# Kernel optimization log

Hardware: AMD Instinct MI355X
Metric: run time of the kernel (lower is better)

The kernel has to match this reference:

```python
import jax, jax.numpy as jnp
import numpy as np


def _ln(x, w, b):
    m = x.mean(-1, keepdims=True)
    v = ((x - m) ** 2).mean(-1, keepdims=True)
    return (x - m) * jax.lax.rsqrt(v + 1e-5) * w + b


def _l2n(x):
    return x / jnp.clip(jnp.linalg.norm(x, axis=-1, keepdims=True), 1e-12, None)


def _forward(tokens, emb, ln1_w, ln1_b, wq, wkv, wo, wo_b, knn_scale,
             ln2_w, ln2_b, ff_w1, ff_b1, ff_w2, ff_b2, lnf_w, lnf_b,
             w_logits, b_logits, xl_mems, db_kv, knn_layer, topk):
    B, N = tokens.shape
    depth = wq.shape[0]
    H = knn_scale.shape[0]
    Dh = wkv.shape[-1] // 2
    XL = xl_mems.shape[2]
    NEG = jnp.finfo(emb.dtype).max
    x = emb[tokens]  # [B,N,dim]
    # causal mask with XL-cache offset: triu(j - i + 1)
    causal = jnp.triu(jnp.ones((N, N + XL), bool), XL + 1)
    for l in range(depth):
        h = _ln(x, ln1_w[l], ln1_b[l])
        q = (h @ wq[l]).reshape(B, N, H, Dh).transpose(0, 2, 1, 3)  # [B,H,N,Dh]
        kv = h @ wkv[l]
        k, v = kv[..., :Dh], kv[..., Dh:]  # single shared kv head [B,N,Dh]
        is_knn = (l == knn_layer)
        if is_knn:
            q, k = _l2n(q), _l2n(k)
            scale = jnp.exp(knn_scale)[None, :, None, None]
        else:
            q = q * (Dh ** -0.5)
            scale = 1.0
        k = jnp.concatenate((xl_mems[l, :, :, 0], k), axis=1)  # [B,N+XL,Dh]
        v = jnp.concatenate((xl_mems[l, :, :, 1], v), axis=1)
        sim = jnp.einsum('bhid,bjd->bhij', q, k) * scale
        sim = jnp.where(causal, -NEG, sim)
        if is_knn:
            dbk = _l2n(db_kv[..., 0, :])  # [B,M,Dh] stored keys are l2-normalized
            dbv = db_kv[..., 1, :]
            simdb = jnp.einsum('bhid,bmd->bhim', q, dbk)
            _, idx = jax.lax.top_k(simdb, topk)  # [B,H,N,topk] inner-product KNN
            mem_k = jax.vmap(lambda t, i: t[i])(dbk, idx)  # [B,H,N,topk,Dh]
            mem_v = jax.vmap(lambda t, i: t[i])(dbv, idx)
            sim_mem = jnp.einsum('bhid,bhijd->bhij', q, mem_k) * scale
            attn = jax.nn.softmax(jnp.concatenate((sim_mem, sim), axis=-1), axis=-1)
            mem_attn, loc_attn = attn[..., :topk], attn[..., topk:]
            out = (jnp.einsum('bhij,bjd->bhid', loc_attn, v)
                   + jnp.einsum('bhij,bhijd->bhid', mem_attn, mem_v))
        else:
            attn = jax.nn.softmax(sim, axis=-1)
            out = jnp.einsum('bhij,bjd->bhid', attn, v)
        out = out.transpose(0, 2, 1, 3).reshape(B, N, H * Dh)
        x = out @ wo[l] + wo_b[l] + x
        h = _ln(x, ln2_w[l], ln2_b[l])
        x = jax.nn.gelu(h @ ff_w1[l] + ff_b1[l], approximate=False) @ ff_w2[l] + ff_b2[l] + x
    return _ln(x, lnf_w, lnf_b) @ w_logits + b_logits


def setup_inputs() -> dict:
    B, N, DIM, H, DH, DEPTH, V, XL, M = 2, 1024, 1024, 16, 64, 4, 32000, 256, 4096
    key = jax.random.key(0)
    ks = jax.random.split(key, 12)
    s = 0.02
    rn = lambda k, sh: (jax.random.normal(k, sh) * s).astype(jnp.float32)
    return dict(
        tokens=jax.random.randint(ks[0], (B, N), 0, V, dtype=jnp.int32),
        emb=rn(ks[1], (V, DIM)),
        ln1_w=jnp.ones((DEPTH, DIM), jnp.float32), ln1_b=jnp.zeros((DEPTH, DIM), jnp.float32),
        wq=rn(ks[2], (DEPTH, DIM, H * DH)),
        wkv=rn(ks[3], (DEPTH, DIM, 2 * DH)),
        wo=rn(ks[4], (DEPTH, H * DH, DIM)), wo_b=jnp.zeros((DEPTH, DIM), jnp.float32),
        knn_scale=jnp.full((H,), float(np.log(20.0)), jnp.float32),
        ln2_w=jnp.ones((DEPTH, DIM), jnp.float32), ln2_b=jnp.zeros((DEPTH, DIM), jnp.float32),
        ff_w1=rn(ks[5], (DEPTH, DIM, 4 * DIM)), ff_b1=jnp.zeros((DEPTH, 4 * DIM), jnp.float32),
        ff_w2=rn(ks[6], (DEPTH, 4 * DIM, DIM)), ff_b2=jnp.zeros((DEPTH, DIM), jnp.float32),
        lnf_w=jnp.ones((DIM,), jnp.float32), lnf_b=jnp.zeros((DIM,), jnp.float32),
        w_logits=rn(ks[7], (DIM, V)), b_logits=jnp.zeros((V,), jnp.float32),
        xl_mems=jax.random.normal(ks[8], (DEPTH, B, XL, 2, DH), jnp.float32),
        db_kv=jax.random.normal(ks[9], (B, M, 2, DH), jnp.float32),
        knn_layer=2, topk=32,
    )


def reference(tokens, emb, ln1_w, ln1_b, wq, wkv, wo, wo_b, knn_scale,
              ln2_w, ln2_b, ff_w1, ff_b1, ff_w2, ff_b2, lnf_w, lnf_b,
              w_logits, b_logits, xl_mems, db_kv, knn_layer, topk):
    return _forward(tokens, emb, ln1_w, ln1_b, wq, wkv, wo, wo_b, knn_scale,
                    ln2_w, ln2_b, ff_w1, ff_b1, ff_w2, ff_b2, lnf_w, lnf_b,
                    w_logits, b_logits, xl_mems, db_kv, knn_layer, topk)
```

## Files before the change

### kernel.cpp

```cpp
#include <hip/hip_runtime.h>
#include <hip/hip_bf16.h>
#include <math.h>

#define BB 2
#define NSEQ 1024
#define DIM 1024
#define NH 16
#define DH 64
#define DEPTH 4
#define VOCAB 32000
#define XLM 256
#define MDB 4096
#define TOPK 32
#define KNN_LAYER 2
#define BNROWS (BB * NSEQ)
#define LOGITS_CHUNK 6400
#define NKEYS 1280
#define KSP_PS ((size_t)BB * NKEYS * DH)

typedef __bf16 bf16x8v __attribute__((ext_vector_type(8)));
typedef float f32x4v __attribute__((ext_vector_type(4)));
typedef unsigned short u16x8v __attribute__((ext_vector_type(8)));

__device__ __forceinline__ float bfbits2f(unsigned short u) {
    union { float f; unsigned int i; } v; v.i = ((unsigned int)u) << 16; return v.f;
}
__device__ __forceinline__ unsigned short f2bfbits(float f) {
    union { __hip_bfloat16 b; unsigned short u; } v;
    v.b = __float2bfloat16(f);
    return v.u;
}
__device__ __forceinline__ float bf2f(__hip_bfloat16 h) { return __bfloat162float(h); }
__device__ __forceinline__ __hip_bfloat16 f2bf(float f) { return __float2bfloat16(f); }

__device__ __forceinline__ void gload16(const void* gp, void* lp) {
    __builtin_amdgcn_global_load_lds(
        (const __attribute__((address_space(1))) unsigned int*)gp,
        (__attribute__((address_space(3))) unsigned int*)lp, 16, 0, 0);
}

__global__ __launch_bounds__(256) void embed_kernel(const int* __restrict__ tok,
                                                    const float* __restrict__ emb,
                                                    float* __restrict__ x) {
    int r = blockIdx.x, t = threadIdx.x;
    int id = tok[r];
    const float* er = emb + (size_t)id * DIM;
    float* xr = x + (size_t)r * DIM;
#pragma unroll
    for (int i = 0; i < 4; i++) xr[t + 256 * i] = er[t + 256 * i];
}

__global__ __launch_bounds__(256) void ln_kernel(const float* __restrict__ x,
                                                 const float* __restrict__ w,
                                                 const float* __restrict__ b,
                                                 __hip_bfloat16* __restrict__ y,
                                                 size_t ypS) {
    __shared__ float red[256];
    int r = blockIdx.x, t = threadIdx.x;
    const float* xr = x + (size_t)r * DIM;
    float v[4];
#pragma unroll
    for (int i = 0; i < 4; i++) v[i] = xr[t + 256 * i];
    float s = v[0] + v[1] + v[2] + v[3];
    red[t] = s; __syncthreads();
    for (int st = 128; st; st >>= 1) { if (t < st) red[t] += red[t + st]; __syncthreads(); }
    float mean = red[0] * (1.0f / DIM);
    __syncthreads();
    float s2 = 0.f;
#pragma unroll
    for (int i = 0; i < 4; i++) { float d = v[i] - mean; s2 += d * d; }
    red[t] = s2; __syncthreads();
    for (int st = 128; st; st >>= 1) { if (t < st) red[t] += red[t + st]; __syncthreads(); }
    float rs = rsqrtf(red[0] * (1.0f / DIM) + 1e-5f);
    __hip_bfloat16* yr = y + (size_t)r * DIM;
#pragma unroll
    for (int i = 0; i < 4; i++) {
        int c = t + 256 * i;
        float val = (v[i] - mean) * rs * w[c] + b[c];
        __hip_bfloat16 hv = f2bf(val);
        yr[c] = hv;
        yr[c + ypS] = f2bf(val - bf2f(hv));
    }
}

__global__ void l2norm_kernel(float* __restrict__ p, int stride) {
    int r = blockIdx.x, t = threadIdx.x;
    float* pr = p + (size_t)r * stride;
    float v = pr[t];
    float s = v * v;
#pragma unroll
    for (int off = 32; off; off >>= 1) s += __shfl_xor(s, off, 64);
    float n = fmaxf(sqrtf(s), 1e-12f);
    pr[t] = v / n;
}

__global__ void dbnorm_kernel(const float* __restrict__ db, float* __restrict__ dbkn) {
    int r = blockIdx.x, t = threadIdx.x;
    float v = db[((size_t)r * 2 + 0) * DH + t];
    float s = v * v;
#pragma unroll
    for (int off = 32; off; off >>= 1) s += __shfl_xor(s, off, 64);
    float n = fmaxf(sqrtf(s), 1e-12f);
    dbkn[(size_t)r * DH + t] = v / n;
}

__global__ __launch_bounds__(256) void split_conv(const float* __restrict__ x,
                                                  unsigned short* __restrict__ y,
                                                  size_t pS, size_t n4) {
    size_t idx = (size_t)blockIdx.x * 256 + threadIdx.x;
    if (idx >= n4) return;
    float4 v = *(const float4*)&x[idx * 4];
    float vv[4] = {v.x, v.y, v.z, v.w};
    ushort4 h4, l4;
    unsigned short* hp = (unsigned short*)&h4;
    unsigned short* lp = (unsigned short*)&l4;
#pragma unroll
    for (int j = 0; j < 4; j++) {
        hp[j] = f2bfbits(vv[j]);
        lp[j] = f2bfbits(vv[j] - bfbits2f(hp[j]));
    }
    *(ushort4*)&y[idx * 4] = h4;
    *(ushort4*)&y[idx * 4 + pS] = l4;
}

template <int NP>
__global__ __launch_bounds__(256) void combine_k(const float* __restrict__ pbuf, size_t pS,
                                                 float* __restrict__ out,
                                                 const float* __restrict__ bias,
                                                 const float* __restrict__ res,
                                                 int N, size_t n4) {
    size_t idx = (size_t)blockIdx.x * 256 + threadIdx.x;
    if (idx >= n4) return;
    f32x4v s = *(const f32x4v*)&pbuf[idx * 4];
#pragma unroll
    for (int z = 1; z < NP; z++) {
        f32x4v v = *(const f32x4v*)&pbuf[(size_t)z * pS + idx * 4];
        s += v;
    }
    if (bias) {
        int col = (int)((idx * 4) % (size_t)N);
        const f32x4v bv = *(const f32x4v*)&bias[col];
        s += bv;
    }
    if (res) {
        f32x4v r = *(const f32x4v*)&res[idx * 4];
        s += r;
    }
    *(f32x4v*)&out[idx * 4] = s;
}

__global__ void kv_prep(const float* __restrict__ kvf, const float* __restrict__ xlm,
                        unsigned short* __restrict__ ksp, unsigned short* __restrict__ vtp) {
    int key = blockIdx.x, b = blockIdx.y, d = threadIdx.x;
    float kvv, vvv;
    if (key < XLM) {
        kvv = xlm[(((size_t)b * XLM + key) * 2 + 0) * DH + d];
        vvv = xlm[(((size_t)b * XLM + key) * 2 + 1) * DH + d];
    } else {
        const float* r = &kvf[(size_t)(b * NSEQ + key - XLM) * 128];
        kvv = r[d]; vvv = r[64 + d];
    }
    unsigned short kh = f2bfbits(kvv), kl = f2bfbits(kvv - bfbits2f(kh));
    unsigned short vh = f2bfbits(vvv), vl = f2bfbits(vvv - bfbits2f(vh));
    size_t ko = (size_t)b * NKEYS * DH + (size_t)key * DH + d;
    ksp[ko] = kh; ksp[ko + KSP_PS] = kl;
    size_t vo = (size_t)b * DH * NKEYS + (size_t)d * NKEYS + key;
    vtp[vo] = vh; vtp[vo + KSP_PS] = vl;
}

__global__ __launch_bounds__(256) void wconv(const float* __restrict__ W,
                                             __hip_bfloat16* __restrict__ WT,
                                             size_t wpS, int K, int N, int ldw,
                                             int wlo) {
    __shared__ float tile[64][65];
    int k0 = blockIdx.x * 64, n0 = blockIdx.y * 64;
    int t = threadIdx.x;
    int r = t >> 4, c4 = (t & 15) * 4;
#pragma unroll
    for (int rr = 0; rr < 4; rr++) {
        int row = rr * 16 + r;
        float4 v = *(const float4*)&W[(size_t)(k0 + row) * ldw + n0 + c4];
        tile[row][c4] = v.x; tile[row][c4 + 1] = v.y; tile[row][c4 + 2] = v.z; tile[row][c4 + 3] = v.w;
    }
    __syncthreads();
#pragma unroll
    for (int rr = 0; rr < 4; rr++) {
        int nrow = rr * 16 + r;
        size_t base = (size_t)(n0 + nrow) * K + k0 + c4;
#pragma unroll
        for (int j = 0; j < 4; j++) {
            float val = tile[c4 + j][nrow];
            __hip_bfloat16 hv = f2bf(val);
            WT[base + j] = hv;
            if (wlo) WT[base + j + wpS] = f2bf(val - bf2f(hv));
        }
    }
}

template <typename OT, int ACT, int TERMS, int MODE>
__global__ __launch_bounds__(256) void gemm_split(const __hip_bfloat16* __restrict__ A, int lda, size_t apS,
                                                  const __hip_bfloat16* __restrict__ BT, int ldb, size_t bpS,
                                                  OT* __restrict__ C, int ldc, size_t cpS, int K,
                                                  const float* __restrict__ bias,
                                                  const float* __restrict__ res,
                                                  int bh0) {
    __shared__ __align__(16) __hip_bfloat16 sAh[128 * 32];
    __shared__ __align__(16) __hip_bfloat16 sBh[128 * 32];
    __shared__ __align__(16) __hip_bfloat16 sAl[TERMS >= 2 ? 128 * 32 : 1];
    __shared__ __align__(16) __hip_bfloat16 sBl[TERMS >= 3 ? 128 * 32 : 1];
    if constexpr (MODE == 1) {
        int bh = bh0 + blockIdx.z;
        A += ((size_t)(bh >> 4) * NSEQ) * lda + (bh & 15) * DH;
        BT += (size_t)(bh >> 4) * MDB * ldb;
        C += (size_t)blockIdx.z * NSEQ * ldc;
    }
    if constexpr (MODE == 2) {
        A += (size_t)blockIdx.z * K;
        BT += (size_t)blockIdx.z * K;
        C += (size_t)blockIdx.z * cpS;
    }
    int bn = blockIdx.x * 128;
    int bm = blockIdx.y * 128;
    int t = threadIdx.x;
    int lane = t & 63, wid = t >> 6;
    int wr = wid >> 1, wc = wid & 1;
    int lr = lane & 15, kc = lane >> 4;

    f32x4v acc[4][4];
#pragma unroll
    for (int m = 0; m < 4; m++)
#pragma unroll
        for (int n = 0; n < 4; n++) acc[m][n] = (f32x4v){0.f, 0.f, 0.f, 0.f};

    for (int k0 = 0; k0 < K; k0 += 32) {
        __syncthreads();
#pragma unroll
        for (int it = 0; it < 2; it++) {
            int e = wid * 128 + it * 64 + lane;
            int r = e >> 2;
            int cl = (e & 3) ^ ((r >> 1) & 3);
            size_t aoff = (size_t)(bm + r) * lda + k0 + cl * 8;
            size_t boff = (size_t)(bn + r) * ldb + k0 + cl * 8;
            int dst = (wid * 128 + it * 64) * 8;
            gload16(&A[aoff], &sAh[dst]);
            gload16(&BT[boff], &sBh[dst]);
            if constexpr (TERMS >= 2) gload16(&A[aoff + apS], &sAl[dst]);
            if constexpr (TERMS >= 3) gload16(&BT[boff + bpS], &sBl[dst]);
        }
        __syncthreads();

        bf16x8v ah[4], al[4], bh[4], bl[4];
#pragma unroll
        for (int m = 0; m < 4; m++) {
            int row = wr * 64 + m * 16 + lr;
            int off = row * 32 + ((kc ^ ((row >> 1) & 3)) << 3);
            ah[m] = *(const bf16x8v*)&sAh[off];
            if constexpr (TERMS >= 2) al[m] = *(const bf16x8v*)&sAl[off];
        }
#pragma unroll
        for (int n = 0; n < 4; n++) {
            int row = wc * 64 + n * 16 + lr;
            int off = row * 32 + ((kc ^ ((row >> 1) & 3)) << 3);
            bh[n] = *(const bf16x8v*)&sBh[off];
            if constexpr (TERMS >= 3) bl[n] = *(const bf16x8v*)&sBl[off];
        }
#pragma unroll
        for (int m = 0; m < 4; m++)
#pragma unroll
            for (int n = 0; n < 4; n++) {
                acc[m][n] = __builtin_amdgcn_mfma_f32_16x16x32_bf16(ah[m], bh[n], acc[m][n], 0, 0, 0);
                if constexpr (TERMS >= 2)
                    acc[m][n] = __builtin_amdgcn_mfma_f32_16x16x32_bf16(al[m], bh[n], acc[m][n], 0, 0, 0);
                if constexpr (TERMS >= 3)
                    acc[m][n] = __builtin_amdgcn_mfma_f32_16x16x32_bf16(ah[m], bl[n], acc[m][n], 0, 0, 0);
            }
    }

#pragma unroll
    for (int m = 0; m < 4; m++) {
#pragma unroll
        for (int n = 0; n < 4; n++) {
            int gcol = bn + wc * 64 + n * 16 + lr;
            float bv = bias ? bias[gcol] : 0.f;
#pragma unroll
            for (int j = 0; j < 4; j++) {
                int grow = bm + wr * 64 + m * 16 + kc * 4 + j;
                float v = acc[m][n][j] + bv;
                if (ACT == 1) v = 0.5f * v * (1.0f + erff(v * 0.70710678118654752f));
                if (res) v += res[(size_t)grow * ldc + gcol];
                size_t idx = (size_t)grow * ldc + gcol;
                if constexpr (__is_same(OT, float)) {
                    C[idx] = v;
                } else if constexpr (__is_same(OT, unsigned short)) {
                    C[idx] = f2bfbits(v);
                } else {
                    __hip_bfloat16 hv = f2bf(v);
                    C[idx] = hv;
                    C[idx + cpS] = f2bf(v - bf2f(hv));
                }
            }
        }
    }
}

template <int KNNL>
__global__ __launch_bounds__(256) void flash_kernel(const float* __restrict__ q,
                                                    const unsigned short* __restrict__ ksp,
                                                    const unsigned short* __restrict__ vtp,
                                                    const float* __restrict__ knn_scale,
                                                    __hip_bfloat16* __restrict__ out,
                                                    size_t opS,
                                                    float* __restrict__ stats) {
    __shared__ __align__(16) unsigned short sKh[64 * 64];
    __shared__ __align__(16) unsigned short sKl[64 * 64];
    __shared__ __align__(16) unsigned short sVh[64 * 64];
    __shared__ __align__(16) unsigned short sVl[64 * 64];
    __shared__ __align__(16) float sPf[4 * 16 * 64];

    int qt = blockIdx.x, h = blockIdx.y, b = blockIdx.z;
    int q0 = qt * 64;
    int t = threadIdx.x;
    int w = t >> 6;
    int lane = t & 63;
    int lr = lane & 15, kc = lane >> 4;
    int wbase = w * 1024;

    float scale = KNNL ? __expf(knn_scale[h]) : 0.125f;

    bf16x8v qh[2], ql[2];
    {
        const float* qbase = q + (size_t)(b * NSEQ + q0 + w * 16 + lr) * DIM + h * DH;
#pragma unroll
        for (int ks = 0; ks < 2; ks++) {
            const float* s = qbase + ks * 32 + kc * 8;
            float4 a = *(const float4*)s;
            float4 c2 = *(const float4*)(s + 4);
            float vv[8] = {a.x, a.y, a.z, a.w, c2.x, c2.y, c2.z, c2.w};
            u16x8v hi, lo;
#pragma unroll
            for (int j = 0; j < 8; j++) {
                hi[j] = f2bfbits(vv[j]);
                lo[j] = f2bfbits(vv[j] - bfbits2f(hi[j]));
            }
            qh[ks] = *(bf16x8v*)&hi;
            ql[ks] = *(bf16x8v*)&lo;
        }
    }

    float m[4], l[4];
    f32x4v o[4];
#pragma unroll
    for (int j = 0; j < 4; j++) { m[j] = -1e30f; l[j] = 0.f; }
#pragma unroll
    for (int f = 0; f < 4; f++) o[f] = (f32x4v){0.f, 0.f, 0.f, 0.f};

    int ntiles = 5 + qt;
    size_t kbase = (size_t)b * NKEYS * DH;
    size_t vbase = (size_t)b * DH * NKEYS;

    for (int T = 0; T < ntiles; T++) {
        __syncthreads();
#pragma unroll
        for (int i2 = 0; i2 < 2; i2++) {
            int cbase = i2 * 256 + w * 64;
            int c = cbase + lane;
            int key = c >> 3, ch = (c & 7) ^ (key & 7);
            size_t ko = kbase + (size_t)(T * 64 + key) * DH + ch * 8;
            gload16(&ksp[ko], &sKh[cbase * 8]);
            gload16(&ksp[ko + KSP_PS], &sKl[cbase * 8]);
            int dim = c >> 3, k8 = (c & 7) ^ (dim & 7);
            size_t vo = vbase + (size_t)dim * NKEYS + T * 64 + k8 * 8;
            gload16(&vtp[vo], &sVh[cbase * 8]);
            gload16(&vtp[vo + KSP_PS], &sVl[cbase * 8]);
        }
        __syncthreads();

        f32x4v s4[4];
#pragma unroll
        for (int n = 0; n < 4; n++) s4[n] = (f32x4v){0.f, 0.f, 0.f, 0.f};
#pragma unroll
        for (int ks = 0; ks < 2; ks++) {
            bf16x8v qh_ = qh[ks], ql_ = ql[ks];
#pragma unroll
            for (int n = 0; n < 4; n++) {
                int row = n * 16 + lr;
                int off = row * 64 + (((ks * 4 + kc) ^ (lr & 7)) << 3);
                bf16x8v kh = *(const bf16x8v*)&sKh[off];
                bf16x8v kl = *(const bf16x8v*)&sKl[off];
                s4[n] = __builtin_amdgcn_mfma_f32_16x16x32_bf16(qh_, kh, s4[n], 0, 0, 0);
                s4[n] = __builtin_amdgcn_mfma_f32_16x16x32_bf16(ql_, kh, s4[n], 0, 0, 0);
                s4[n] = __builtin_amdgcn_mfma_f32_16x16x32_bf16(qh_, kl, s4[n], 0, 0, 0);
            }
        }

#pragma unroll
        for (int n = 0; n < 4; n++) {
            int key = T * 64 + n * 16 + lr;
#pragma unroll
            for (int j = 0; j < 4; j++) {
                int gq = q0 + w * 16 + kc * 4 + j;
                float sv = s4[n][j] * scale;
                s4[n][j] = (key <= XLM + gq) ? sv : -1e30f;
            }
        }

        float tm[4];
#pragma unroll
        for (int j = 0; j < 4; j++) {
            float v = fmaxf(fmaxf(s4[0][j], s4[1][j]), fmaxf(s4[2][j], s4[3][j]));
            v = fmaxf(v, __shfl_xor(v, 1, 64));
            v = fmaxf(v, __shfl_xor(v, 2, 64));
            v = fmaxf(v, __shfl_xor(v, 4, 64));
            v = fmaxf(v, __shfl_xor(v, 8, 64));
            tm[j] = v;
        }
        float alpha[4];
#pragma unroll
        for (int j = 0; j < 4; j++) {
            float mnew = fmaxf(m[j], tm[j]);
            alpha[j] = __expf(m[j] - mnew);
            m[j] = mnew;
        }
        float psum[4] = {0.f, 0.f, 0.f, 0.f};
#pragma unroll
        for (int n = 0; n < 4; n++)
#pragma unroll
            for (int j = 0; j < 4; j++) {
                float p = __expf(s4[n][j] - m[j]);
                s4[n][j] = p;
                psum[j] += p;
            }
#pragma unroll
        for (int j = 0; j < 4; j++) {
            float v = psum[j];
            v += __shfl_xor(v, 1, 64);
            v += __shfl_xor(v, 2, 64);
            v += __shfl_xor(v, 4, 64);
            v += __shfl_xor(v, 8, 64);
            l[j] = l[j] * alpha[j] + v;
        }
#pragma unroll
        for (int f = 0; f < 4; f++)
#pragma unroll
            for (int j = 0; j < 4; j++) o[f][j] *= alpha[j];

#pragma unroll
        for (int n = 0; n < 4; n++) {
            int chunkcol = 2 * n + (lr >> 3);
#pragma unroll
            for (int j = 0; j < 4; j++) {
                int row = kc * 4 + j;
                int off = wbase + row * 64 + (((chunkcol ^ (row & 7)) << 3) + (lr & 7));
                sPf[off] = s4[n][j];
            }
        }

#pragma unroll
        for (int ks = 0; ks < 2; ks++) {
            int poff = wbase + lr * 64 + (((ks * 4 + kc) ^ (lr & 7)) << 3);
            float4 a = *(const float4*)&sPf[poff];
            float4 c2 = *(const float4*)&sPf[poff + 4];
            float vv[8] = {a.x, a.y, a.z, a.w, c2.x, c2.y, c2.z, c2.w};
            u16x8v hib, lob;
#pragma unroll
            for (int j = 0; j < 8; j++) {
                hib[j] = f2bfbits(vv[j]);
                lob[j] = f2bfbits(vv[j] - bfbits2f(hib[j]));
            }
            bf16x8v ph = *(bf16x8v*)&hib;
            bf16x8v pl = *(bf16x8v*)&lob;
#pragma unroll
            for (int f = 0; f < 4; f++) {
                int row = f * 16 + lr;
                int off = row * 64 + (((ks * 4 + kc) ^ (lr & 7)) << 3);
                bf16x8v vh = *(const bf16x8v*)&sVh[off];
                bf16x8v vl = *(const bf16x8v*)&sVl[off];
                o[f] = __builtin_amdgcn_mfma_f32_16x16x32_bf16(ph, vh, o[f], 0, 0, 0);
                o[f] = __builtin_amdgcn_mfma_f32_16x16x32_bf16(pl, vh, o[f], 0, 0, 0);
                o[f] = __builtin_amdgcn_mfma_f32_16x16x32_bf16(ph, vl, o[f], 0, 0, 0);
            }
        }
    }

    float inv[4];
#pragma unroll
    for (int j = 0; j < 4; j++) inv[j] = 1.0f / l[j];
    unsigned short* outu = (unsigned short*)out;
#pragma unroll
    for (int f = 0; f < 4; f++)
#pragma unroll
        for (int j = 0; j < 4; j++) {
            int gq = q0 + w * 16 + kc * 4 + j;
            size_t oidx = (size_t)(b * NSEQ + gq) * DIM + h * DH + f * 16 + lr;
            float v = o[f][j] * inv[j];
            unsigned short hv = f2bfbits(v);
            outu[oidx] = hv;
            outu[oidx + opS] = f2bfbits(v - bfbits2f(hv));
        }
    if (KNNL && lr == 0) {
#pragma unroll
        for (int j = 0; j < 4; j++) {
            int gq = q0 + w * 16 + kc * 4 + j;
            size_t srow = (((size_t)b * NH + h) * NSEQ + gq) * 2;
            stats[srow] = m[j];
            stats[srow + 1] = l[j];
        }
    }
}

__global__ __launch_bounds__(256) void knn_select(const unsigned short* __restrict__ simdb,
                                                  const float* __restrict__ db,
                                                  const float* __restrict__ qf,
                                                  const float* __restrict__ dbkn,
                                                  const float* __restrict__ knn_scale,
                                                  const float* __restrict__ stats,
                                                  __hip_bfloat16* __restrict__ out,
                                                  size_t opS,
                                                  int bh0) {
    __shared__ unsigned short sv[4 * 4096];

    int bh = bh0 + blockIdx.y;
    int b = bh >> 4, h = bh & 15;
    int t = threadIdx.x;
    int w = t >> 6, lane = t & 63;
    int i = blockIdx.x * 4 + w;
    unsigned short* svw = &sv[w * 4096];

    const unsigned short* srow = &simdb[((size_t)blockIdx.y * NSEQ + i) * MDB];
#pragma unroll
    for (int it = 0; it < 8; it++) {
        int g = it * 64 + lane;
        int c = g >> 3, sub = g & 7;
        u16x8v d = *(const u16x8v*)&srow[(size_t)g * 8];
        *(u16x8v*)&svw[c * 64 + ((sub ^ (c & 7)) << 3)] = d;
    }

    float lmax = -1e30f; int lidx = 0;
#pragma unroll
    for (int c = 0; c < 64; c++) {
        float v = bfbits2f(svw[c * 64 + (lane ^ ((c & 7) << 3))]);
        if (v > lmax) { lmax = v; lidx = c * 64 + lane; }
    }

    int tidx = 0;
    for (int it = 0; it < TOPK; it++) {
        float v = lmax; int idx = lidx;
#pragma unroll
        for (int off = 32; off; off >>= 1) {
            float v2 = __shfl_xor(v, off, 64);
            int i2 = __shfl_xor(idx, off, 64);
            if (v2 > v || (v2 == v && i2 < idx)) { v = v2; idx = i2; }
        }
        if (lane == it) tidx = idx;
        int col = idx & 63, cc = idx >> 6;
        if (lane == 0) svw[cc * 64 + (col ^ ((cc & 7) << 3))] = 0xFF80;
        float rv = bfbits2f(svw[lane * 64 + (col ^ ((lane & 7) << 3))]);
        int ridx = lane * 64 + col;
#pragma unroll
        for (int off = 32; off; off >>= 1) {
            float v2 = __shfl_xor(rv, off, 64);
            int i2 = __shfl_xor(ridx, off, 64);
            if (v2 > rv || (v2 == rv && i2 < ridx)) { rv = v2; ridx = i2; }
        }
        if (lane == col) { lmax = rv; lidx = ridx; }
    }

    float srec = -1e30f;
    if (lane < TOPK) {
        const float* qrow = &qf[(size_t)(b * NSEQ + i) * DIM + h * DH];
        const float* krow = &dbkn[((size_t)b * MDB + tidx) * DH];
        float s = 0.f;
#pragma unroll
        for (int d4 = 0; d4 < 16; d4++) {
            float4 a = *(const float4*)&qrow[d4 * 4];
            float4 k2 = *(const float4*)&krow[d4 * 4];
            s += a.x * k2.x + a.y * k2.y + a.z * k2.z + a.w * k2.w;
        }
        srec = s;
    }

    float scl = __expf(knn_scale[h]);
    size_t srow_idx = (((size_t)b * NH + h) * NSEQ + i) * 2;
    float m_loc = stats[srow_idx], l_loc = stats[srow_idx + 1];
    float mm = srec;
#pragma unroll
    for (int off = 32; off; off >>= 1) mm = fmaxf(mm, __shfl_xor(mm, off, 64));
    float M = fmaxf(m_loc, mm * scl);
    float co = __expf(m_loc - M);
    float e = (lane < TOPK) ? __expf(srec * scl - M) : 0.f;
    float esum = e;
#pragma unroll
    for (int off = 32; off; off >>= 1) esum += __shfl_xor(esum, off, 64);
    float denom = l_loc * co + esum;

    float acc = 0.f;
#pragma unroll
    for (int j = 0; j < TOPK; j++) {
        int idxj = __shfl(tidx, j, 64);
        float ej = __shfl(e, j, 64);
        acc += ej * db[(((size_t)b * MDB + idxj) * 2 + 1) * DH + lane];
    }

    size_t op = (size_t)(b * NSEQ + i) * DIM + h * DH + lane;
    float o_loc = bf2f(out[op]) + bf2f(out[op + opS]);
    float nv = (o_loc * l_loc * co + acc) / denom;
    __hip_bfloat16 hv = f2bf(nv);
    out[op] = hv;
    out[op + opS] = f2bf(nv - bf2f(hv));
}

extern "C" void kernel_launch(void* const* d_in, const int* in_sizes, int n_in,
                              void* d_out, int out_size, void* d_ws, size_t ws_size,
                              hipStream_t stream) {
    const int* tokens = (const int*)d_in[0];
    const float* emb = (const float*)d_in[1];
    const float* ln1_w = (const float*)d_in[2];
    const float* ln1_b = (const float*)d_in[3];
    const float* wq = (const float*)d_in[4];
    const float* wkv = (const float*)d_in[5];
    const float* wo = (const float*)d_in[6];
    const float* wo_b = (const float*)d_in[7];
    const float* knn_scale = (const float*)d_in[8];
    const float* ln2_w = (const float*)d_in[9];
    const float* ln2_b = (const float*)d_in[10];
    const float* ff_w1 = (const float*)d_in[11];
    const float* ff_b1 = (const float*)d_in[12];
    const float* ff_w2 = (const float*)d_in[13];
    const float* ff_b2 = (const float*)d_in[14];
    const float* lnf_w = (const float*)d_in[15];
    const float* lnf_b = (const float*)d_in[16];
    const float* w_logits = (const float*)d_in[17];
    const float* b_logits = (const float*)d_in[18];
    const float* xl_mems = (const float*)d_in[19];
    const float* db_kv = (const float*)d_in[20];

    const size_t PS_H = (size_t)BNROWS * DIM;
    char* p = (char*)d_ws;
    float* x = (float*)p;                p += PS_H * 4;
    __hip_bfloat16* hb = (__hip_bfloat16*)p;  p += PS_H * 2 * 2;
    float* qf = (float*)p;               p += PS_H * 4;
    float* kvf = (float*)p;              p += (size_t)BNROWS * 128 * 4;
    float* dbkn = (float*)p;             p += (size_t)BB * MDB * DH * 4;
    float* stats = (float*)p;            p += (size_t)BB * NH * NSEQ * 2 * 4;
    unsigned short* ksp = (unsigned short*)p; p += KSP_PS * 2 * 2;
    unsigned short* vtp = (unsigned short*)p; p += KSP_PS * 2 * 2;
    __hip_bfloat16* wT = (__hip_bfloat16*)p; p += (size_t)4096 * DIM * 2 * 2;

    unsigned short* qsplit = (unsigned short*)wT;
    unsigned short* dbks = (unsigned short*)wT + 2 * PS_H;
    const size_t PS_DB = (size_t)BB * MDB * DH;

    const size_t PS_MID = (size_t)BNROWS * 4 * DIM;
    __hip_bfloat16* midb = (__hip_bfloat16*)d_out;
    float* logits = (float*)d_out;
    float* part = (float*)((char*)d_out + ((size_t)64 << 20));

    embed_kernel<<<BNROWS, 256, 0, stream>>>(tokens, emb, x);
    dbnorm_kernel<<<BB * MDB, 64, 0, stream>>>(db_kv, dbkn);

    for (int l = 0; l < DEPTH; l++) {
        const float* wq_l = wq + (size_t)l * DIM * DIM;
        const float* wkv_l = wkv + (size_t)l * DIM * 128;
        const float* wo_l = wo + (size_t)l * DIM * DIM;
        const float* xlm_l = xl_mems + (size_t)l * BB * XLM * 2 * DH;

        ln_kernel<<<BNROWS, 256, 0, stream>>>(x, ln1_w + (size_t)l * DIM, ln1_b + (size_t)l * DIM, hb, PS_H);

        wconv<<<dim3(16, 16), 256, 0, stream>>>(wq_l, wT, (size_t)DIM * DIM, DIM, DIM, DIM, 1);
        gemm_split<float, 0, 3, 2><<<dim3(DIM / 128, BNROWS / 128, 2), 256, 0, stream>>>(
            hb, DIM, PS_H, wT, DIM, (size_t)DIM * DIM, part, DIM, PS_H, 512, nullptr, nullptr, 0);
        combine_k<2><<<(PS_H / 4 + 255) / 256, 256, 0, stream>>>(
            part, PS_H, qf, nullptr, nullptr, DIM, PS_H / 4);
        wconv<<<dim3(16, 2), 256, 0, stream>>>(wkv_l, wT, (size_t)128 * DIM, DIM, 128, 128, 1);
        gemm_split<float, 0, 3, 2><<<dim3(1, BNROWS / 128, 8), 256, 0, stream>>>(
            hb, DIM, PS_H, wT, DIM, (size_t)128 * DIM, part, 128, (size_t)BNROWS * 128, 128, nullptr, nullptr, 0);
        combine_k<8><<<((size_t)BNROWS * 128 / 4 + 255) / 256, 256, 0, stream>>>(
            part, (size_t)BNROWS * 128, kvf, nullptr, nullptr, 128, (size_t)BNROWS * 128 / 4);

        if (l == KNN_LAYER) {
            l2norm_kernel<<<BNROWS * NH, 64, 0, stream>>>(qf, DH);
            l2norm_kernel<<<BNROWS, 64, 0, stream>>>(kvf, 128);
            kv_prep<<<dim3(NKEYS, BB), 64, 0, stream>>>(kvf, xlm_l, ksp, vtp);
            split_conv<<<(PS_H / 4 + 255) / 256, 256, 0, stream>>>(qf, qsplit, PS_H, PS_H / 4);
            split_conv<<<(PS_DB / 4 + 255) / 256, 256, 0, stream>>>(dbkn, dbks, PS_DB, PS_DB / 4);
            flash_kernel<1><<<dim3(NSEQ / 64, NH, BB), 256, 0, stream>>>(
                qf, ksp, vtp, knn_scale, hb, PS_H, stats);
            const int CHUNK = 8;
            for (int bh0 = 0; bh0 < BB * NH; bh0 += CHUNK) {
                gemm_split<unsigned short, 0, 3, 1><<<dim3(MDB / 128, NSEQ / 128, CHUNK), 256, 0, stream>>>(
                    (const __hip_bfloat16*)qsplit, DIM, PS_H,
                    (const __hip_bfloat16*)dbks, DH, PS_DB,
                    (unsigned short*)d_out, MDB, 0, DH, nullptr, nullptr, bh0);
                knn_select<<<dim3(NSEQ / 4, CHUNK), 256, 0, stream>>>(
                    (const unsigned short*)d_out, db_kv, qf, dbkn, knn_scale, stats, hb, PS_H, bh0);
            }
        } else {
            kv_prep<<<dim3(NKEYS, BB), 64, 0, stream>>>(kvf, xlm_l, ksp, vtp);
            flash_kernel<0><<<dim3(NSEQ / 64, NH, BB), 256, 0, stream>>>(
                qf, ksp, vtp, knn_scale, hb, PS_H, stats);
        }

        wconv<<<dim3(16, 16), 256, 0, stream>>>(wo_l, wT, (size_t)DIM * DIM, DIM, DIM, DIM, 1);
        gemm_split<float, 0, 3, 2><<<dim3(DIM / 128, BNROWS / 128, 2), 256, 0, stream>>>(
            hb, DIM, PS_H, wT, DIM, (size_t)DIM * DIM, part, DIM, PS_H, 512, nullptr, nullptr, 0);
        combine_k<2><<<(PS_H / 4 + 255) / 256, 256, 0, stream>>>(
            part, PS_H, x, wo_b + (size_t)l * DIM, x, DIM, PS_H / 4);

        ln_kernel<<<BNROWS, 256, 0, stream>>>(x, ln2_w + (size_t)l * DIM, ln2_b + (size_t)l * DIM, hb, PS_H);
        wconv<<<dim3(16, 64), 256, 0, stream>>>(ff_w1 + (size_t)l * DIM * 4 * DIM, wT, (size_t)4096 * DIM, DIM, 4 * DIM, 4 * DIM, 1);
        gemm_split<__hip_bfloat16, 1, 3, 0><<<dim3(4 * DIM / 128, BNROWS / 128), 256, 0, stream>>>(
            hb, DIM, PS_H, wT, DIM, (size_t)4096 * DIM, midb, 4 * DIM, PS_MID, DIM,
            ff_b1 + (size_t)l * 4 * DIM, nullptr, 0);
        wconv<<<dim3(64, 16), 256, 0, stream>>>(ff_w2 + (size_t)l * 4 * DIM * DIM, wT, (size_t)DIM * 4096, 4 * DIM, DIM, DIM, 1);
        gemm_split<float, 0, 3, 2><<<dim3(DIM / 128, BNROWS / 128, 2), 256, 0, stream>>>(
            midb, 4 * DIM, PS_MID, wT, 4 * DIM, (size_t)DIM * 4096, part, DIM, PS_H, 2048, nullptr, nullptr, 0);
        combine_k<2><<<(PS_H / 4 + 255) / 256, 256, 0, stream>>>(
            part, PS_H, x, ff_b2 + (size_t)l * DIM, x, DIM, PS_H / 4);
    }

    ln_kernel<<<BNROWS, 256, 0, stream>>>(x, lnf_w, lnf_b, hb, PS_H);
    for (int c0 = 0; c0 < VOCAB; c0 += LOGITS_CHUNK) {
        wconv<<<dim3(16, LOGITS_CHUNK / 64), 256, 0, stream>>>(
            w_logits + c0, wT, 0, DIM, LOGITS_CHUNK, VOCAB, 0);
        gemm_split<float, 0, 1, 0><<<dim3(LOGITS_CHUNK / 128, BNROWS / 128), 256, 0, stream>>>(
            hb, DIM, PS_H, wT, DIM, 0, logits + c0, VOCAB, 0, DIM,
            b_logits + c0, nullptr, 0);
    }
}
```

Baseline: 2.315 ms.

## Fuse residual combine with LayerNorm and raise split-K for small-grid GEMMs

Adds a combine_ln kernel that sums the split-K partials, adds the bias and residual, and applies the next LayerNorm in a single pass, so the separate ln_kernel launches and their extra reads of x are gone. The Q, KV, Wo and FF2 GEMMs get a higher split-K factor so more workgroups cover the device. The FF1 GEMM now runs split-K with float partials, and a new combine kernel applies bias, GELU and the bf16 hi/lo split. The trade-off is more partial-buffer traffic: FF1 now writes float partials for the 4*DIM-wide output, and the partial scratch region in d_out is moved to make room for them.

```diff
diff --git a/kernel.cpp b/kernel.cpp
--- a/kernel.cpp
+++ b/kernel.cpp
@@ -83,6 +83,49 @@
     }
 }
 
+template <int NP>
+__global__ __launch_bounds__(256) void combine_ln(const float* __restrict__ pbuf, size_t pS,
+                                                  const float* __restrict__ bias,
+                                                  float* __restrict__ x,
+                                                  const float* __restrict__ w,
+                                                  const float* __restrict__ b,
+                                                  __hip_bfloat16* __restrict__ y,
+                                                  size_t ypS) {
+    __shared__ float red[256];
+    int r = blockIdx.x, t = threadIdx.x;
+    float v[4];
+#pragma unroll
+    for (int i = 0; i < 4; i++) {
+        int c = t + 256 * i;
+        size_t idx = (size_t)r * DIM + c;
+        float s = bias[c] + x[idx];
+#pragma unroll
+        for (int z = 0; z < NP; z++) s += pbuf[(size_t)z * pS + idx];
+        v[i] = s;
+        x[idx] = s;
+    }
+    float s = v[0] + v[1] + v[2] + v[3];
+    red[t] = s; __syncthreads();
+    for (int st = 128; st; st >>= 1) { if (t < st) red[t] += red[t + st]; __syncthreads(); }
+    float mean = red[0] * (1.0f / DIM);
+    __syncthreads();
+    float s2 = 0.f;
+#pragma unroll
+    for (int i = 0; i < 4; i++) { float d = v[i] - mean; s2 += d * d; }
+    red[t] = s2; __syncthreads();
+    for (int st = 128; st; st >>= 1) { if (t < st) red[t] += red[t + st]; __syncthreads(); }
+    float rs = rsqrtf(red[0] * (1.0f / DIM) + 1e-5f);
+    __hip_bfloat16* yr = y + (size_t)r * DIM;
+#pragma unroll
+    for (int i = 0; i < 4; i++) {
+        int c = t + 256 * i;
+        float val = (v[i] - mean) * rs * w[c] + b[c];
+        __hip_bfloat16 hv = f2bf(val);
+        yr[c] = hv;
+        yr[c + ypS] = f2bf(val - bf2f(hv));
+    }
+}
+
 __global__ void l2norm_kernel(float* __restrict__ p, int stride) {
     int r = blockIdx.x, t = threadIdx.x;
     float* pr = p + (size_t)r * stride;
@@ -147,6 +190,36 @@
         s += r;
     }
     *(f32x4v*)&out[idx * 4] = s;
+}
+
+template <int NP>
+__global__ __launch_bounds__(256) void combine_gelu_split(const float* __restrict__ pbuf, size_t pS,
+                                                          const float* __restrict__ bias, int N,
+                                                          unsigned short* __restrict__ y, size_t ypS,
+                                                          size_t n4) {
+    size_t idx = (size_t)blockIdx.x * 256 + threadIdx.x;
+    if (idx >= n4) return;
+    f32x4v s = *(const f32x4v*)&pbuf[idx * 4];
+#pragma unroll
+    for (int z = 1; z < NP; z++) {
+        f32x4v v = *(const f32x4v*)&pbuf[(size_t)z * pS + idx * 4];
+        s += v;
+    }
+    int col = (int)((idx * 4) % (size_t)N);
+    const f32x4v bv = *(const f32x4v*)&bias[col];
+    s += bv;
+    ushort4 h4, l4;
+    unsigned short* hp = (unsigned short*)&h4;
+    unsigned short* lp = (unsigned short*)&l4;
+#pragma unroll
+    for (int j = 0; j < 4; j++) {
+        float v = s[j];
+        v = 0.5f * v * (1.0f + erff(v * 0.70710678118654752f));
+        hp[j] = f2bfbits(v);
+        lp[j] = f2bfbits(v - bfbits2f(hp[j]));
+    }
+    *(ushort4*)&y[idx * 4] = h4;
+    *(ushort4*)&y[idx * 4 + ypS] = l4;
 }
 
 __global__ void kv_prep(const float* __restrict__ kvf, const float* __restrict__ xlm,
@@ -653,10 +726,11 @@
     const size_t PS_MID = (size_t)BNROWS * 4 * DIM;
     __hip_bfloat16* midb = (__hip_bfloat16*)d_out;
     float* logits = (float*)d_out;
-    float* part = (float*)((char*)d_out + ((size_t)64 << 20));
+    float* part = (float*)((char*)d_out + ((size_t)96 << 20));
 
     embed_kernel<<<BNROWS, 256, 0, stream>>>(tokens, emb, x);
     dbnorm_kernel<<<BB * MDB, 64, 0, stream>>>(db_kv, dbkn);
+    ln_kernel<<<BNROWS, 256, 0, stream>>>(x, ln1_w, ln1_b, hb, PS_H);
 
     for (int l = 0; l < DEPTH; l++) {
         const float* wq_l = wq + (size_t)l * DIM * DIM;
@@ -664,17 +738,15 @@
         const float* wo_l = wo + (size_t)l * DIM * DIM;
         const float* xlm_l = xl_mems + (size_t)l * BB * XLM * 2 * DH;
 
-        ln_kernel<<<BNROWS, 256, 0, stream>>>(x, ln1_w + (size_t)l * DIM, ln1_b + (size_t)l * DIM, hb, PS_H);
-
         wconv<<<dim3(16, 16), 256, 0, stream>>>(wq_l, wT, (size_t)DIM * DIM, DIM, DIM, DIM, 1);
-        gemm_split<float, 0, 3, 2><<<dim3(DIM / 128, BNROWS / 128, 2), 256, 0, stream>>>(
-            hb, DIM, PS_H, wT, DIM, (size_t)DIM * DIM, part, DIM, PS_H, 512, nullptr, nullptr, 0);
-        combine_k<2><<<(PS_H / 4 + 255) / 256, 256, 0, stream>>>(
+        gemm_split<float, 0, 3, 2><<<dim3(DIM / 128, BNROWS / 128, 4), 256, 0, stream>>>(
+            hb, DIM, PS_H, wT, DIM, (size_t)DIM * DIM, part, DIM, PS_H, 256, nullptr, nullptr, 0);
+        combine_k<4><<<(PS_H / 4 + 255) / 256, 256, 0, stream>>>(
             part, PS_H, qf, nullptr, nullptr, DIM, PS_H / 4);
         wconv<<<dim3(16, 2), 256, 0, stream>>>(wkv_l, wT, (size_t)128 * DIM, DIM, 128, 128, 1);
-        gemm_split<float, 0, 3, 2><<<dim3(1, BNROWS / 128, 8), 256, 0, stream>>>(
-            hb, DIM, PS_H, wT, DIM, (size_t)128 * DIM, part, 128, (size_t)BNROWS * 128, 128, nullptr, nullptr, 0);
-        combine_k<8><<<((size_t)BNROWS * 128 / 4 + 255) / 256, 256, 0, stream>>>(
+        gemm_split<float, 0, 3, 2><<<dim3(1, BNROWS / 128, 16), 256, 0, stream>>>(
+            hb, DIM, PS_H, wT, DIM, (size_t)128 * DIM, part, 128, (size_t)BNROWS * 128, 64, nullptr, nullptr, 0);
+        combine_k<16><<<((size_t)BNROWS * 128 / 4 + 255) / 256, 256, 0, stream>>>(
             part, (size_t)BNROWS * 128, kvf, nullptr, nullptr, 128, (size_t)BNROWS * 128 / 4);
 
         if (l == KNN_LAYER) {
@@ -701,24 +773,28 @@
         }
 
         wconv<<<dim3(16, 16), 256, 0, stream>>>(wo_l, wT, (size_t)DIM * DIM, DIM, DIM, DIM, 1);
-        gemm_split<float, 0, 3, 2><<<dim3(DIM / 128, BNROWS / 128, 2), 256, 0, stream>>>(
-            hb, DIM, PS_H, wT, DIM, (size_t)DIM * DIM, part, DIM, PS_H, 512, nullptr, nullptr, 0);
-        combine_k<2><<<(PS_H / 4 + 255) / 256, 256, 0, stream>>>(
-            part, PS_H, x, wo_b + (size_t)l * DIM, x, DIM, PS_H / 4);
-
-        ln_kernel<<<BNROWS, 256, 0, stream>>>(x, ln2_w + (size_t)l * DIM, ln2_b + (size_t)l * DIM, hb, PS_H);
+        gemm_split<float, 0, 3, 2><<<dim3(DIM / 128, BNROWS / 128, 4), 256, 0, stream>>>(
+            hb, DIM, PS_H, wT, DIM, (size_t)DIM * DIM, part, DIM, PS_H, 256, nullptr, nullptr, 0);
+        combine_ln<4><<<BNROWS, 256, 0, stream>>>(
+            part, PS_H, wo_b + (size_t)l * DIM, x,
+            ln2_w + (size_t)l * DIM, ln2_b + (size_t)l * DIM, hb, PS_H);
+
         wconv<<<dim3(16, 64), 256, 0, stream>>>(ff_w1 + (size_t)l * DIM * 4 * DIM, wT, (size_t)4096 * DIM, DIM, 4 * DIM, 4 * DIM, 1);
-        gemm_split<__hip_bfloat16, 1, 3, 0><<<dim3(4 * DIM / 128, BNROWS / 128), 256, 0, stream>>>(
-            hb, DIM, PS_H, wT, DIM, (size_t)4096 * DIM, midb, 4 * DIM, PS_MID, DIM,
-            ff_b1 + (size_t)l * 4 * DIM, nullptr, 0);
+        gemm_split<float, 0, 3, 2><<<dim3(4 * DIM / 128, BNROWS / 128, 2), 256, 0, stream>>>(
+            hb, DIM, PS_H, wT, DIM, (size_t)4096 * DIM, part, 4 * DIM, PS_MID, 512, nullptr, nullptr, 0);
+        combine_gelu_split<2><<<(PS_MID / 4 + 255) / 256, 256, 0, stream>>>(
+            part, PS_MID, ff_b1 + (size_t)l * 4 * DIM, 4 * DIM,
+            (unsigned short*)midb, PS_MID, PS_MID / 4);
+
         wconv<<<dim3(64, 16), 256, 0, stream>>>(ff_w2 + (size_t)l * 4 * DIM * DIM, wT, (size_t)DIM * 4096, 4 * DIM, DIM, DIM, 1);
-        gemm_split<float, 0, 3, 2><<<dim3(DIM / 128, BNROWS / 128, 2), 256, 0, stream>>>(
-            midb, 4 * DIM, PS_MID, wT, 4 * DIM, (size_t)DIM * 4096, part, DIM, PS_H, 2048, nullptr, nullptr, 0);
-        combine_k<2><<<(PS_H / 4 + 255) / 256, 256, 0, stream>>>(
-            part, PS_H, x, ff_b2 + (size_t)l * DIM, x, DIM, PS_H / 4);
-    }
-
-    ln_kernel<<<BNROWS, 256, 0, stream>>>(x, lnf_w, lnf_b, hb, PS_H);
+        gemm_split<float, 0, 3, 2><<<dim3(DIM / 128, BNROWS / 128, 4), 256, 0, stream>>>(
+            midb, 4 * DIM, PS_MID, wT, 4 * DIM, (size_t)DIM * 4096, part, DIM, PS_H, 1024, nullptr, nullptr, 0);
+        const float* nw = (l < DEPTH - 1) ? ln1_w + (size_t)(l + 1) * DIM : lnf_w;
+        const float* nb = (l < DEPTH - 1) ? ln1_b + (size_t)(l + 1) * DIM : lnf_b;
+        combine_ln<4><<<BNROWS, 256, 0, stream>>>(
+            part, PS_H, ff_b2 + (size_t)l * DIM, x, nw, nb, hb, PS_H);
+    }
+
     for (int c0 = 0; c0 < VOCAB; c0 += LOGITS_CHUNK) {
         wconv<<<dim3(16, LOGITS_CHUNK / 64), 256, 0, stream>>>(
             w_logits + c0, wT, 0, DIM, LOGITS_CHUNK, VOCAB, 0);
```

New measurement: 2.276 ms. No clear change (-1.7%).
